# Kernel tuning notes

Hardware: AMD Instinct MI355X
Metric: run time of the kernel (lower is better)

The kernel has to match this reference:

```python
import jax, jax.numpy as jnp
import numpy as np

EPS = 1e-8

def setup_inputs() -> dict:
    key = jax.random.key(0)
    ks = jax.random.split(key, 4)
    B, N, D = 16, 2048, 1024
    APP = 1024
    x = jax.random.normal(ks[0], (B, N, D), dtype=jnp.float32)
    mask = jax.random.uniform(ks[1], (N, B), dtype=jnp.float32)  # [N, B] per original
    Wp = jax.random.normal(ks[2], (1024, D), dtype=jnp.float32) * 0.02
    bp = jnp.zeros((1024,), dtype=jnp.float32)
    Wv = jax.random.normal(ks[3], (APP, D), dtype=jnp.float32) * 0.02
    bv = jnp.zeros((APP,), dtype=jnp.float32)
    return {"x": x, "mask": mask, "Wp": Wp, "bp": bp, "Wv": Wv, "bv": bv}

def reference(x, mask, Wp, bp, Wv, bv):
    # proj + ReLU: [B,N,1024]
    xp = jax.nn.relu(jnp.einsum('bnd,pd->bnp', x, Wp) + bp)
    # L2-normalize along feature dim (matches xp / (norm + eps))
    xp = xp / (jnp.linalg.norm(xp, axis=2, keepdims=True) + EPS)
    # mask: [N,B] -> [B,N] (transpose+reshape in original yields [B,1,N])
    m = mask.T  # [B, N]
    # att_i = sum_j m_j * <xp_i, xp_j> / sum_j m_j  == <xp_i, sum_j m_j xp_j> / sum_j m_j
    ws = jnp.einsum('bn,bnp->bp', m, xp)                # [B, 1024]
    att = jnp.einsum('bnp,bp->bn', xp, ws) / jnp.sum(m, axis=1, keepdims=True)  # [B, N]
    # value + ReLU: [B,N,APP]
    xv = jax.nn.relu(jnp.einsum('bnd,ad->bna', x, Wv) + bv)
    return att[:, :, None] * xv
```

## Files before the change

kernel.cpp:

```cpp
#include <hip/hip_runtime.h>

#define B_  16
#define N_  2048
#define D_  1024
#define P_  1024
#define M_  (B_*N_)

typedef __attribute__((ext_vector_type(8))) short bf16x8;
typedef __attribute__((ext_vector_type(4))) float f32x4;

__device__ __forceinline__ float bf2f(unsigned short u) {
    union { unsigned int i; float f; } v; v.i = ((unsigned int)u) << 16; return v.f;
}
__device__ __forceinline__ unsigned short f2bf(float f) {
    union { unsigned int i; float f; } v; v.f = f;
    unsigned int i = v.i;
    return (unsigned short)((i + 0x7FFFu + ((i >> 16) & 1u)) >> 16);
}

__device__ __forceinline__ void async_cp16(const void* g, void* s) {
    __builtin_amdgcn_global_load_lds((const __attribute__((address_space(1))) void*)g,
                                     (__attribute__((address_space(3))) void*)s,
                                     16, 0, 0);
}

__global__ void cvt_all_k(const float* __restrict__ x,  unsigned short* __restrict__ xb,
                          const float* __restrict__ Wp, unsigned short* __restrict__ Wpb,
                          const float* __restrict__ Wv, unsigned short* __restrict__ Wvb)
{
    const int stride = gridDim.x * 256 * 4;
    const int base = (blockIdx.x * 256 + threadIdx.x) * 4;
    for (int i = base; i < M_ * D_; i += stride) {
        float4 v = *(const float4*)(x + i);
        union { unsigned short u[4]; unsigned long long ll; } p;
        p.u[0]=f2bf(v.x); p.u[1]=f2bf(v.y); p.u[2]=f2bf(v.z); p.u[3]=f2bf(v.w);
        *(unsigned long long*)(xb + i) = p.ll;
    }
    for (int i = base; i < P_ * D_; i += stride) {
        float4 v = *(const float4*)(Wp + i);
        union { unsigned short u[4]; unsigned long long ll; } p;
        p.u[0]=f2bf(v.x); p.u[1]=f2bf(v.y); p.u[2]=f2bf(v.z); p.u[3]=f2bf(v.w);
        *(unsigned long long*)(Wpb + i) = p.ll;
    }
    for (int i = base; i < P_ * D_; i += stride) {
        float4 v = *(const float4*)(Wv + i);
        union { unsigned short u[4]; unsigned long long ll; } p;
        p.u[0]=f2bf(v.x); p.u[1]=f2bf(v.y); p.u[2]=f2bf(v.z); p.u[3]=f2bf(v.w);
        *(unsigned long long*)(Wvb + i) = p.ll;
    }
}

template<int MODE>
__global__ __launch_bounds__(512, 2) void gemm8p(const unsigned short* __restrict__ A,
                                                 const unsigned short* __restrict__ W,
                                                 const float* __restrict__ bias,
                                                 const float* __restrict__ att,
                                                 void* __restrict__ Cv)
{
    __shared__ unsigned short smem[65536];

    const int id  = blockIdx.x;
    const int xcd = id & 7, idx = id >> 3;
    const int bx  = idx & 3;
    const int by  = xcd * 16 + (idx >> 2);
    const int m0  = by << 8, p0 = bx << 8;

    const int t    = threadIdx.x;
    const int lane = t & 63, wave = t >> 6;
    const int wr   = wave >> 2, wc = wave & 3;
    const int lr   = lane & 15, lq = lane >> 4;

    const int aBase = (wr * 64 + lr) * 64;
    const int bBase = (wc * 32 + lr) * 64;
    const int c0 = ((lq       ^ (lr & 7)) & 7) * 8;
    const int c1 = (((lq | 4) ^ (lr & 7)) & 7) * 8;

    const int srowT = t >> 3;
    const int slot8 = (t & 7) * 8;
    const int lch8  = (((t & 7) ^ (srowT & 7)) & 7) * 8;
    const unsigned short* Ag = A + ((size_t)m0 << 10) + lch8;
    const unsigned short* Bg = W + ((size_t)p0 << 10) + lch8;

    auto stageA = [&](int buf, int rb, int tt) {
        const unsigned short* s = Ag + ((size_t)(rb + srowT) << 10) + (tt << 6);
        async_cp16(s,                      smem + buf * 16384 + (rb + srowT) * 64 + slot8);
        async_cp16(s + ((size_t)64 << 10), smem + buf * 16384 + (rb + 64 + srowT) * 64 + slot8);
    };
    auto stageB = [&](int buf, int rb, int tt) {
        const unsigned short* s = Bg + ((size_t)(rb + srowT) << 10) + (tt << 6);
        async_cp16(s,                      smem + 32768 + buf * 16384 + (rb + srowT) * 64 + slot8);
        async_cp16(s + ((size_t)64 << 10), smem + 32768 + buf * 16384 + (rb + 64 + srowT) * 64 + slot8);
    };

    f32x4 acc[8][4];
    #pragma unroll
    for (int i = 0; i < 8; ++i)
        #pragma unroll
        for (int j = 0; j < 4; ++j) acc[i][j] = (f32x4){0.f, 0.f, 0.f, 0.f};

    stageA(0, 0, 0); stageA(0, 128, 0); stageB(0, 0, 0); stageB(0, 128, 0);
    stageA(1, 0, 1); stageA(1, 128, 1); stageB(1, 0, 1); stageB(1, 128, 1);
    asm volatile("s_waitcnt vmcnt(8)" ::: "memory");
    __builtin_amdgcn_sched_barrier(0);
    __builtin_amdgcn_s_barrier();

#define VMW4 do { asm volatile("s_waitcnt vmcnt(4)" ::: "memory"); \
                  __builtin_amdgcn_sched_barrier(0); } while (0)
#define NOVM ((void)0)
#define PHASE(BUFC, MH, NH, STAGE_STMT, DO_VM) do {                                   \
    bf16x8 afr[4][2], bfr[2][2];                                                      \
    const unsigned short* Ab_ = smem + (BUFC) * 16384 + (MH) * 8192 + aBase;          \
    const unsigned short* Bb_ = smem + 32768 + (BUFC) * 16384 + (NH) * 8192 + bBase;  \
    _Pragma("unroll")                                                                 \
    for (int i_ = 0; i_ < 4; ++i_) {                                                  \
        afr[i_][0] = *(const bf16x8*)(Ab_ + i_ * 1024 + c0);                          \
        afr[i_][1] = *(const bf16x8*)(Ab_ + i_ * 1024 + c1);                          \
    }                                                                                 \
    _Pragma("unroll")                                                                 \
    for (int j_ = 0; j_ < 2; ++j_) {                                                  \
        bfr[j_][0] = *(const bf16x8*)(Bb_ + j_ * 1024 + c0);                          \
        bfr[j_][1] = *(const bf16x8*)(Bb_ + j_ * 1024 + c1);                          \
    }                                                                                 \
    STAGE_STMT;                                                                       \
    __builtin_amdgcn_s_barrier();                                                     \
    asm volatile("s_waitcnt lgkmcnt(0)" ::: "memory");                                \
    __builtin_amdgcn_sched_barrier(0);                                                \
    __builtin_amdgcn_s_setprio(1);                                                    \
    _Pragma("unroll")                                                                 \
    for (int h_ = 0; h_ < 2; ++h_)                                                    \
        _Pragma("unroll")                                                             \
        for (int i_ = 0; i_ < 4; ++i_)                                                \
            _Pragma("unroll")                                                         \
            for (int j_ = 0; j_ < 2; ++j_)                                            \
                acc[(MH) * 4 + i_][(NH) * 2 + j_] =                                   \
                    __builtin_amdgcn_mfma_f32_16x16x32_bf16(                          \
                        afr[i_][h_], bfr[j_][h_],                                     \
                        acc[(MH) * 4 + i_][(NH) * 2 + j_], 0, 0, 0);                  \
    __builtin_amdgcn_s_setprio(0);                                                    \
    DO_VM;                                                                            \
    __builtin_amdgcn_s_barrier();                                                     \
} while (0)

    #pragma unroll 1
    for (int it = 0; it < 8; ++it) {
        const int t1 = 2 * it + 1;
        const int t2 = (2 * it + 2) & 15;
        const int t3 = (2 * it + 3) & 15;
        PHASE(0, 0, 0, { if (it) stageA(1, 128, t1); }, NOVM);
        PHASE(0, 1, 0, { if (it) stageB(1, 128, t1); }, NOVM);
        PHASE(0, 0, 1, stageB(0, 0,   t2), NOVM);
        PHASE(0, 1, 1, stageA(0, 0,   t2), VMW4);
        PHASE(1, 0, 0, stageA(0, 128, t2), NOVM);
        PHASE(1, 1, 0, stageB(0, 128, t2), NOVM);
        PHASE(1, 0, 1, stageB(1, 0,   t3), NOVM);
        PHASE(1, 1, 1, stageA(1, 0,   t3), VMW4);
    }
#undef PHASE
#undef VMW4
#undef NOVM

    asm volatile("s_waitcnt vmcnt(0)" ::: "memory");
    __syncthreads();

    if (MODE == 0) {
        float bi[4];
        #pragma unroll
        for (int nj = 0; nj < 4; ++nj)
            bi[nj] = bias[p0 + ((nj >> 1) << 7) + wc * 32 + ((nj & 1) << 4) + lr];
        unsigned short* Cp = (unsigned short*)Cv;
        #pragma unroll
        for (int mh = 0; mh < 2; ++mh) {
            #pragma unroll
            for (int i = 0; i < 4; ++i) {
                const int rl = wr * 64 + i * 16 + lq * 4;
                #pragma unroll
                for (int nj = 0; nj < 4; ++nj) {
                    const int colL = ((nj >> 1) << 7) + wc * 32 + ((nj & 1) << 4) + lr;
                    #pragma unroll
                    for (int v = 0; v < 4; ++v) {
                        const float val = fmaxf(acc[mh * 4 + i][nj][v] + bi[nj], 0.f);
                        smem[(rl + v) * 256 + colL] = f2bf(val);
                    }
                }
            }
            __syncthreads();
            #pragma unroll
            for (int pas = 0; pas < 8; ++pas) {
                const int ix = pas * 512 + t;
                const int row = ix >> 5, ch = ix & 31;
                bf16x8 vv = *(const bf16x8*)(smem + row * 256 + ch * 8);
                *(bf16x8*)(Cp + (size_t)(m0 + mh * 128 + row) * P_ + p0 + ch * 8) = vv;
            }
            __syncthreads();
        }
    } else {
        float* Cp = (float*)Cv;
        #pragma unroll
        for (int mi = 0; mi < 8; ++mi) {
            const int row = m0 + ((mi >> 2) << 7) + wr * 64 + ((mi & 3) << 4) + lq * 4;
            float av[4];
            #pragma unroll
            for (int v = 0; v < 4; ++v) av[v] = att[row + v];
            #pragma unroll
            for (int nj = 0; nj < 4; ++nj) {
                const int col = p0 + ((nj >> 1) << 7) + wc * 32 + ((nj & 1) << 4) + lr;
                const float b0v = bias[col];
                #pragma unroll
                for (int v = 0; v < 4; ++v) {
                    const float val = fmaxf(acc[mi][nj][v] + b0v, 0.f);
                    Cp[(size_t)(row + v) * P_ + col] = val * av[v];
                }
            }
        }
    }
}

template<int MODE>
__global__ __launch_bounds__(256) void gemm_f32(const float* __restrict__ A,
                                                const float* __restrict__ W,
                                                const float* __restrict__ bias,
                                                const float* __restrict__ att,
                                                void* __restrict__ Cv)
{
    const int K = D_, BK = 32;
    __shared__ float As[128 * 32];
    __shared__ float Bs[128 * 32];
    const int id = blockIdx.x;
    const int bx = (id >> 3) & 7;
    const int by = ((id >> 6) << 3) | (id & 7);
    const int m0 = by * 128, p0 = bx * 128;
    const int wave = threadIdx.x >> 6, lane = threadIdx.x & 63;
    const int wr = wave >> 1, wc = wave & 1;
    const int srow = wave * 32 + (lane >> 3);
    const int scol = (lane & 7) * 4;
    const float* ag = A + (size_t)(m0 + srow) * K + scol;
    const float* bg = W + (size_t)(p0 + srow) * K + scol;
    float* as = &As[srow * BK + scol];
    float* bs = &Bs[srow * BK + scol];
    f32x4 acc[4][4];
    #pragma unroll
    for (int i = 0; i < 4; i++)
        #pragma unroll
        for (int j = 0; j < 4; j++) acc[i][j] = (f32x4){0.f,0.f,0.f,0.f};
    const int lr = lane & 15, lq = lane >> 4;
    const float* Ar = &As[(wr * 64 + lr) * BK + lq * 8];
    const float* Br = &Bs[(wc * 64 + lr) * BK + lq * 8];
    for (int kb = 0; kb < K; kb += BK) {
        #pragma unroll
        for (int s = 0; s < 4; s++) {
            async_cp16(ag + (size_t)s * 8 * K + kb, as + s * 8 * BK);
            async_cp16(bg + (size_t)s * 8 * K + kb, bs + s * 8 * BK);
        }
        __syncthreads();
        bf16x8 af[4], bf[4];
        #pragma unroll
        for (int i = 0; i < 4; i++) {
            f32x4 a0 = *(const f32x4*)(Ar + i * 16 * BK);
            f32x4 a1 = *(const f32x4*)(Ar + i * 16 * BK + 4);
            #pragma unroll
            for (int e = 0; e < 4; e++) {
                union { float f; unsigned int u; } c;
                c.f = a0[e]; af[i][e]     = (short)(c.u >> 16);
                c.f = a1[e]; af[i][e + 4] = (short)(c.u >> 16);
            }
        }
        #pragma unroll
        for (int j = 0; j < 4; j++) {
            f32x4 b0 = *(const f32x4*)(Br + j * 16 * BK);
            f32x4 b1 = *(const f32x4*)(Br + j * 16 * BK + 4);
            #pragma unroll
            for (int e = 0; e < 4; e++) {
                union { float f; unsigned int u; } c;
                c.f = b0[e]; bf[j][e]     = (short)(c.u >> 16);
                c.f = b1[e]; bf[j][e + 4] = (short)(c.u >> 16);
            }
        }
        #pragma unroll
        for (int i = 0; i < 4; i++)
            #pragma unroll
            for (int j = 0; j < 4; j++)
                acc[i][j] = __builtin_amdgcn_mfma_f32_16x16x32_bf16(af[i], bf[j], acc[i][j], 0, 0, 0);
        __syncthreads();
    }
    const int crow0 = m0 + wr * 64 + lq * 4;
    const int ccol0 = p0 + wc * 64 + lr;
    #pragma unroll
    for (int i = 0; i < 4; i++) {
        float attv[4];
        if (MODE == 1) {
            #pragma unroll
            for (int v = 0; v < 4; v++) attv[v] = att[crow0 + i * 16 + v];
        }
        #pragma unroll
        for (int j = 0; j < 4; j++) {
            const int col = ccol0 + j * 16;
            const float bi = bias[col];
            #pragma unroll
            for (int v = 0; v < 4; v++) {
                const int row = crow0 + i * 16 + v;
                float val = fmaxf(acc[i][j][v] + bi, 0.0f);
                if (MODE == 0) ((unsigned short*)Cv)[(size_t)row * P_ + col] = f2bf(val);
                else           ((float*)Cv)[(size_t)row * P_ + col] = val * attv[v];
            }
        }
    }
}

__global__ __launch_bounds__(256) void fused_nc_k(const unsigned short* __restrict__ X1,
                                                  const float* __restrict__ mask,
                                                  float* __restrict__ inv,
                                                  float* __restrict__ wsv,
                                                  float* __restrict__ msum)
{
    __shared__ float accw[4][1024];
    __shared__ float mred[4];
    const int b = blockIdx.y, nc = blockIdx.x;
    const int wave = threadIdx.x >> 6, lane = threadIdx.x & 63;
    float acc[16];
    #pragma unroll
    for (int e = 0; e < 16; e++) acc[e] = 0.f;
    float msub = 0.f;
    const int rbase = b * N_ + nc * 64 + wave * 16;
    const int nbase = nc * 64 + wave * 16;
    for (int t = 0; t < 16; t++) {
        const int r = rbase + t;
        const unsigned short* row = X1 + (size_t)r * P_;
        bf16x8 u0 = *(const bf16x8*)(row + lane * 16);
        bf16x8 u1 = *(const bf16x8*)(row + lane * 16 + 8);
        float v[16], s = 0.f;
        #pragma unroll
        for (int e = 0; e < 8; e++) { v[e] = bf2f((unsigned short)u0[e]); s += v[e]*v[e]; }
        #pragma unroll
        for (int e = 0; e < 8; e++) { v[8+e] = bf2f((unsigned short)u1[e]); s += v[8+e]*v[8+e]; }
        #pragma unroll
        for (int off = 32; off > 0; off >>= 1) s += __shfl_down(s, off);
        s = __shfl(s, 0);
        const float iv = 1.f / (sqrtf(s) + 1e-8f);
        const float mk = mask[(nbase + t) * B_ + b];
        if (lane == 0) { inv[r] = iv; msub += mk; }
        const float w = mk * iv;
        #pragma unroll
        for (int e = 0; e < 16; e++) acc[e] += w * v[e];
    }
    #pragma unroll
    for (int e = 0; e < 16; e++) accw[wave][e * 64 + lane] = acc[e];
    if (lane == 0) mred[wave] = msub;
    __syncthreads();
    #pragma unroll
    for (int q = 0; q < 4; q++) {
        const int p = threadIdx.x * 4 + q;
        const int col = (p & 63) * 16 + (p >> 6);
        float ssum = accw[0][p] + accw[1][p] + accw[2][p] + accw[3][p];
        atomicAdd(&wsv[b * P_ + col], ssum);
    }
    if (threadIdx.x == 0) atomicAdd(&msum[b], mred[0] + mred[1] + mred[2] + mred[3]);
}

__global__ void att_k(const unsigned short* __restrict__ X1,
                      const float* __restrict__ wsvec,
                      const float* __restrict__ inv,
                      const float* __restrict__ msum,
                      float* __restrict__ att)
{
    const int r = blockIdx.x * 4 + (threadIdx.x >> 6);
    const int lane = threadIdx.x & 63;
    const int b = r >> 11;
    const unsigned short* row = X1 + (size_t)r * P_;
    const float* w = wsvec + b * P_;
    bf16x8 u0 = *(const bf16x8*)(row + lane * 8);
    bf16x8 u1 = *(const bf16x8*)(row + 512 + lane * 8);
    float s = 0.f;
    #pragma unroll
    for (int k = 0; k < 8; k++) s += bf2f((unsigned short)u0[k]) * w[lane * 8 + k];
    #pragma unroll
    for (int k = 0; k < 8; k++) s += bf2f((unsigned short)u1[k]) * w[512 + lane * 8 + k];
    #pragma unroll
    for (int off = 32; off > 0; off >>= 1) s += __shfl_down(s, off);
    if (lane == 0) att[r] = s * inv[r] / msum[b];
}

extern "C" void kernel_launch(void* const* d_in, const int* in_sizes, int n_in,
                              void* d_out, int out_size, void* d_ws, size_t ws_size,
                              hipStream_t stream)
{
    const float* x    = (const float*)d_in[0];
    const float* mask = (const float*)d_in[1];
    const float* Wp   = (const float*)d_in[2];
    const float* bp   = (const float*)d_in[3];
    const float* Wv   = (const float*)d_in[4];
    const float* bv   = (const float*)d_in[5];
    float* out = (float*)d_out;

    unsigned short* X1 = (unsigned short*)d_out;

    const size_t xb_bytes = (size_t)M_ * D_ * 2;
    const size_t wb_bytes = (size_t)P_ * D_ * 2;
    const size_t f_bytes  = 2 * (size_t)M_ * 4 + (size_t)B_ * P_ * 4 + 64;
    const bool big_ws = ws_size >= xb_bytes + 2 * wb_bytes + f_bytes;

    char* ws = (char*)d_ws;
    size_t off = 0;
    unsigned short *xb = nullptr, *Wpb = nullptr, *Wvb = nullptr;
    if (big_ws) {
        xb  = (unsigned short*)(ws + off); off += xb_bytes;
        Wpb = (unsigned short*)(ws + off); off += wb_bytes;
        Wvb = (unsigned short*)(ws + off); off += wb_bytes;
    }
    float* inv  = (float*)(ws + off); off += (size_t)M_ * 4;
    float* att  = (float*)(ws + off); off += (size_t)M_ * 4;
    float* wsv  = (float*)(ws + off); off += (size_t)B_ * P_ * 4;
    float* msum = (float*)(ws + off); off += 64;

    hipMemsetAsync(wsv, 0, (size_t)B_ * P_ * 4 + 64, stream);

    if (big_ws) {
        cvt_all_k<<<2048, 256, 0, stream>>>(x, xb, Wp, Wpb, Wv, Wvb);
        gemm8p<0><<<512, 512, 0, stream>>>(xb, Wpb, bp, nullptr, X1);
    } else {
        const int gblocks = (P_ / 128) * (M_ / 128);
        gemm_f32<0><<<gblocks, 256, 0, stream>>>(x, Wp, bp, nullptr, X1);
    }
    fused_nc_k<<<dim3(32, B_), 256, 0, stream>>>(X1, mask, inv, wsv, msum);
    att_k<<<M_ / 4, 256, 0, stream>>>(X1, wsv, inv, msum, att);
    if (big_ws) gemm8p<1><<<512, 512, 0, stream>>>(xb, Wvb, bv, att, out);
    else {
        const int gblocks = (P_ / 128) * (M_ / 128);
        gemm_f32<1><<<gblocks, 256, 0, stream>>>(x, Wv, bv, att, out);
    }
}
```

Before: 415.3 us.

## Reuse LDS fragments across GEMM phases, split norm kernel finer, vectorize att loads

```diff
diff --git a/kernel.cpp b/kernel.cpp
--- a/kernel.cpp
+++ b/kernel.cpp
@@ -98,6 +98,9 @@
         #pragma unroll
         for (int j = 0; j < 4; ++j) acc[i][j] = (f32x4){0.f, 0.f, 0.f, 0.f};
 
+    bf16x8 aR[2][4][2];
+    bf16x8 bR[2][2];
+
     stageA(0, 0, 0); stageA(0, 128, 0); stageB(0, 0, 0); stageB(0, 128, 0);
     stageA(1, 0, 1); stageA(1, 128, 1); stageB(1, 0, 1); stageB(1, 128, 1);
     asm volatile("s_waitcnt vmcnt(8)" ::: "memory");
@@ -107,19 +110,22 @@
 #define VMW4 do { asm volatile("s_waitcnt vmcnt(4)" ::: "memory"); \
                   __builtin_amdgcn_sched_barrier(0); } while (0)
 #define NOVM ((void)0)
-#define PHASE(BUFC, MH, NH, STAGE_STMT, DO_VM) do {                                   \
-    bf16x8 afr[4][2], bfr[2][2];                                                      \
-    const unsigned short* Ab_ = smem + (BUFC) * 16384 + (MH) * 8192 + aBase;          \
-    const unsigned short* Bb_ = smem + 32768 + (BUFC) * 16384 + (NH) * 8192 + bBase;  \
-    _Pragma("unroll")                                                                 \
-    for (int i_ = 0; i_ < 4; ++i_) {                                                  \
-        afr[i_][0] = *(const bf16x8*)(Ab_ + i_ * 1024 + c0);                          \
-        afr[i_][1] = *(const bf16x8*)(Ab_ + i_ * 1024 + c1);                          \
+#define PHASE(BUFC, MH, NH, RD_A, RD_B, STAGE_STMT, DO_VM) do {                       \
+    if (RD_A) {                                                                       \
+        const unsigned short* Ab_ = smem + (BUFC) * 16384 + (MH) * 8192 + aBase;      \
+        _Pragma("unroll")                                                             \
+        for (int i_ = 0; i_ < 4; ++i_) {                                              \
+            aR[MH][i_][0] = *(const bf16x8*)(Ab_ + i_ * 1024 + c0);                   \
+            aR[MH][i_][1] = *(const bf16x8*)(Ab_ + i_ * 1024 + c1);                   \
+        }                                                                             \
     }                                                                                 \
-    _Pragma("unroll")                                                                 \
-    for (int j_ = 0; j_ < 2; ++j_) {                                                  \
-        bfr[j_][0] = *(const bf16x8*)(Bb_ + j_ * 1024 + c0);                          \
-        bfr[j_][1] = *(const bf16x8*)(Bb_ + j_ * 1024 + c1);                          \
+    if (RD_B) {                                                                       \
+        const unsigned short* Bb_ = smem + 32768 + (BUFC) * 16384 + (NH) * 8192 + bBase; \
+        _Pragma("unroll")                                                             \
+        for (int j_ = 0; j_ < 2; ++j_) {                                              \
+            bR[j_][0] = *(const bf16x8*)(Bb_ + j_ * 1024 + c0);                       \
+            bR[j_][1] = *(const bf16x8*)(Bb_ + j_ * 1024 + c1);                       \
+        }                                                                             \
     }                                                                                 \
     STAGE_STMT;                                                                       \
     __builtin_amdgcn_s_barrier();                                                     \
@@ -134,7 +140,7 @@
             for (int j_ = 0; j_ < 2; ++j_)                                            \
                 acc[(MH) * 4 + i_][(NH) * 2 + j_] =                                   \
                     __builtin_amdgcn_mfma_f32_16x16x32_bf16(                          \
-                        afr[i_][h_], bfr[j_][h_],                                     \
+                        aR[MH][i_][h_], bR[j_][h_],                                   \
                         acc[(MH) * 4 + i_][(NH) * 2 + j_], 0, 0, 0);                  \
     __builtin_amdgcn_s_setprio(0);                                                    \
     DO_VM;                                                                            \
@@ -146,14 +152,14 @@
         const int t1 = 2 * it + 1;
         const int t2 = (2 * it + 2) & 15;
         const int t3 = (2 * it + 3) & 15;
-        PHASE(0, 0, 0, { if (it) stageA(1, 128, t1); }, NOVM);
-        PHASE(0, 1, 0, { if (it) stageB(1, 128, t1); }, NOVM);
-        PHASE(0, 0, 1, stageB(0, 0,   t2), NOVM);
-        PHASE(0, 1, 1, stageA(0, 0,   t2), VMW4);
-        PHASE(1, 0, 0, stageA(0, 128, t2), NOVM);
-        PHASE(1, 1, 0, stageB(0, 128, t2), NOVM);
-        PHASE(1, 0, 1, stageB(1, 0,   t3), NOVM);
-        PHASE(1, 1, 1, stageA(1, 0,   t3), VMW4);
+        PHASE(0, 0, 0, 1, 1, { if (it) stageA(1, 128, t1); }, NOVM);
+        PHASE(0, 1, 0, 1, 0, { if (it) stageB(1, 128, t1); }, NOVM);
+        PHASE(0, 1, 1, 0, 1, stageB(0, 0,   t2), NOVM);
+        PHASE(0, 0, 1, 0, 0, stageA(0, 0,   t2), VMW4);
+        PHASE(1, 0, 0, 1, 1, stageA(0, 128, t2), NOVM);
+        PHASE(1, 1, 0, 1, 0, stageB(0, 128, t2), NOVM);
+        PHASE(1, 1, 1, 0, 1, stageB(1, 0,   t3), NOVM);
+        PHASE(1, 0, 1, 0, 0, stageA(1, 0,   t3), VMW4);
     }
 #undef PHASE
 #undef VMW4
@@ -320,9 +326,9 @@
     #pragma unroll
     for (int e = 0; e < 16; e++) acc[e] = 0.f;
     float msub = 0.f;
-    const int rbase = b * N_ + nc * 64 + wave * 16;
-    const int nbase = nc * 64 + wave * 16;
-    for (int t = 0; t < 16; t++) {
+    const int rbase = b * N_ + nc * 32 + wave * 8;
+    const int nbase = nc * 32 + wave * 8;
+    for (int t = 0; t < 8; t++) {
         const int r = rbase + t;
         const unsigned short* row = X1 + (size_t)r * P_;
         bf16x8 u0 = *(const bf16x8*)(row + lane * 16);
@@ -369,11 +375,19 @@
     const float* w = wsvec + b * P_;
     bf16x8 u0 = *(const bf16x8*)(row + lane * 8);
     bf16x8 u1 = *(const bf16x8*)(row + 512 + lane * 8);
+    f32x4 w0 = *(const f32x4*)(w + lane * 8);
+    f32x4 w1 = *(const f32x4*)(w + lane * 8 + 4);
+    f32x4 w2 = *(const f32x4*)(w + 512 + lane * 8);
+    f32x4 w3 = *(const f32x4*)(w + 512 + lane * 8 + 4);
     float s = 0.f;
     #pragma unroll
-    for (int k = 0; k < 8; k++) s += bf2f((unsigned short)u0[k]) * w[lane * 8 + k];
-    #pragma unroll
-    for (int k = 0; k < 8; k++) s += bf2f((unsigned short)u1[k]) * w[512 + lane * 8 + k];
+    for (int k = 0; k < 4; k++) s += bf2f((unsigned short)u0[k]) * w0[k];
+    #pragma unroll
+    for (int k = 0; k < 4; k++) s += bf2f((unsigned short)u0[k + 4]) * w1[k];
+    #pragma unroll
+    for (int k = 0; k < 4; k++) s += bf2f((unsigned short)u1[k]) * w2[k];
+    #pragma unroll
+    for (int k = 0; k < 4; k++) s += bf2f((unsigned short)u1[k + 4]) * w3[k];
     #pragma unroll
     for (int off = 32; off > 0; off >>= 1) s += __shfl_down(s, off);
     if (lane == 0) att[r] = s * inv[r] / msum[b];
@@ -420,7 +434,7 @@
         const int gblocks = (P_ / 128) * (M_ / 128);
         gemm_f32<0><<<gblocks, 256, 0, stream>>>(x, Wp, bp, nullptr, X1);
     }
-    fused_nc_k<<<dim3(32, B_), 256, 0, stream>>>(X1, mask, inv, wsv, msum);
+    fused_nc_k<<<dim3(64, B_), 256, 0, stream>>>(X1, mask, inv, wsv, msum);
     att_k<<<M_ / 4, 256, 0, stream>>>(X1, wsv, inv, msum, att);
     if (big_ws) gemm8p<1><<<512, 512, 0, stream>>>(xb, Wvb, bv, att, out);
     else {
```

Measured after the change: 410.2 us. About the same (-1.2%).
